# Kernel tuning notes

Hardware: AMD Instinct MI355X
Metric: run time of the kernel (lower is better)

The kernel has to match this reference:

```python
import jax, jax.numpy as jnp
import numpy as np

B, T, P, D, H = 4, 12, 196, 512, 8
DH = D // H
EPS = 1e-6


def _norm(x, alpha, bias):
    # torch Norm: alpha*(x-mean)/(std_unbiased+eps)+bias, std uses Bessel correction (ddof=1)
    mu = jnp.mean(x, axis=-1, keepdims=True)
    sd = jnp.std(x, axis=-1, ddof=1, keepdims=True)
    return alpha * (x - mu) / (sd + EPS) + bias


def setup_inputs() -> dict:
    key = jax.random.key(0)
    ks = jax.random.split(key, 12)
    s = 0.02

    def n(k, shape, scale=s):
        return jax.random.normal(k, shape, jnp.float32) * scale

    return {
        "x": jax.random.normal(ks[0], (B, T, P, D), jnp.float32),
        "Wq": n(ks[1], (D, D)), "bq": jnp.zeros((D,), jnp.float32),
        "Wk": n(ks[2], (D, D)), "bk": jnp.zeros((D,), jnp.float32),
        "Wv": n(ks[3], (D, D)), "bv": jnp.zeros((D,), jnp.float32),
        "in_a": jnp.ones((D,), jnp.float32), "in_b": jnp.zeros((D,), jnp.float32),
        "attn_a": jnp.ones((D,), jnp.float32), "attn_b": jnp.zeros((D,), jnp.float32),
        "out_a": jnp.ones((D,), jnp.float32), "out_b": jnp.zeros((D,), jnp.float32),
        "Wt": n(ks[4], (T, D, D)), "bt": jnp.zeros((T, D), jnp.float32),
        "pos": n(ks[5], (T, T, P, D), 0.02),
        "W1": n(ks[6], (2 * D, D)), "b1": jnp.zeros((2 * D,), jnp.float32),
        "W2": n(ks[7], (D, 2 * D)), "b2": jnp.zeros((D,), jnp.float32),
    }


def reference(x, Wq, bq, Wk, bk, Wv, bv, in_a, in_b, attn_a, attn_b,
              out_a, out_b, Wt, bt, pos, W1, b1, W2, b2):
    x2 = _norm(x, in_a, in_b)

    def proj(W, b):
        # [B,T,P,D] -> [B,T,H,P,DH]
        return (x2 @ W.T + b).reshape(B, T, P, H, DH).transpose(0, 1, 3, 2, 4)

    Q = proj(Wq, bq)
    K = proj(Wk, bk)
    V = proj(Wv, bv)

    # all-pairs temporal cross attention: [B,t,u,H,Pq,Pk]
    qk = jnp.einsum('btijk,builk->btuijl', Q, K) / np.sqrt(DH)
    attn = jax.nn.softmax(qk, axis=-1)  # no mask, dropout=0
    av = jnp.einsum('btuijl,builk->btuijk', attn, V)  # [B,t,u,H,P,DH]
    av = av.transpose(0, 1, 2, 4, 3, 5).reshape(B, T, T, P, D)
    av = _norm(av, attn_a, attn_b)
    x2p = av + pos  # pos broadcasts over batch

    # per-u Linear fused as one batched contraction, summed over u
    tc = jnp.einsum('btupd,ued->btpe', x2p / T, Wt) + jnp.sum(bt, axis=0)
    x = x + jax.nn.gelu(tc, approximate=False)

    x2 = _norm(x, out_a, out_b)
    h = jax.nn.gelu(x2 @ W1.T + b1, approximate=False)
    y = jax.nn.gelu(h @ W2.T + b2, approximate=False)
    return x + y
```

## Files before the change

kernel.cpp:

```cpp
#include <hip/hip_runtime.h>
#include <hip/hip_bf16.h>

typedef __hip_bfloat16 bf16;

typedef __bf16 bfrag8 __attribute__((ext_vector_type(8)));
typedef __bf16 bfrag4 __attribute__((ext_vector_type(4)));
typedef float  ffrag4 __attribute__((ext_vector_type(4)));
typedef float  ffrag16 __attribute__((ext_vector_type(16)));

#define EPS 1e-6f

__device__ __forceinline__ float gelu_exact(float v) {
  return 0.5f * v * (1.0f + erff(v * 0.7071067811865475f));
}

__device__ __forceinline__ void async16(const void* g, void* s) {
  __builtin_amdgcn_global_load_lds(
      (const __attribute__((address_space(1))) unsigned int*)g,
      (__attribute__((address_space(3))) unsigned int*)s, 16, 0, 0);
}

struct alignas(16) bf16x8 { bf16 v[8]; };
struct alignas(4)  bf16p2 { __bf16 v[2]; };

__global__ __launch_bounds__(256) void zero_acc_kernel(float* __restrict__ p) {
  size_t i = ((size_t)blockIdx.x * 256 + threadIdx.x) * 4;
  *(float4*)(p + i) = make_float4(0.f, 0.f, 0.f, 0.f);
}

__global__ __launch_bounds__(256) void conv_w_kernel(
    const float* __restrict__ Wq, const float* __restrict__ Wk,
    const float* __restrict__ Wv, const float* __restrict__ W1,
    const float* __restrict__ W2, const float* __restrict__ Wt,
    __bf16* __restrict__ dst)
{
  size_t e = ((size_t)blockIdx.x * 256 + threadIdx.x) * 8;
  const float* src; size_t off, dsto;
  if      (e <  262144) { src = Wq; off = e;           dsto = e; }
  else if (e <  524288) { src = Wk; off = e -  262144; dsto = e; }
  else if (e <  786432) { src = Wv; off = e -  524288; dsto = e; }
  else if (e < 1310720) { src = W1; off = e -  786432; dsto = e; }
  else if (e < 1835008) { src = W2; off = e - 1310720; dsto = e; }
  else if (e < 4980736) {
    src = Wt; off = e - 1835008;
    size_t u = off >> 18;
    size_t rem = off & 262143;
    size_t eo = rem >> 9, d = rem & 511;
    dsto = 1835008 + eo * 6144 + u * 512 + d;
  }
  else return;
  float4 f0 = *(const float4*)(src + off);
  float4 f1 = *(const float4*)(src + off + 4);
  bfrag8 o;
  o[0] = (__bf16)f0.x; o[1] = (__bf16)f0.y; o[2] = (__bf16)f0.z; o[3] = (__bf16)f0.w;
  o[4] = (__bf16)f1.x; o[5] = (__bf16)f1.y; o[6] = (__bf16)f1.z; o[7] = (__bf16)f1.w;
  *(bfrag8*)(dst + dsto) = o;
}

__global__ __launch_bounds__(512) void sum_bt_kernel(
    const float* __restrict__ bt, float* __restrict__ sbt)
{
  int n = threadIdx.x;
  float s = 0.f;
#pragma unroll
  for (int u = 0; u < 12; ++u) s += bt[u * 512 + n];
  sbt[n] = s;
}

__global__ __launch_bounds__(64) void norm_f32_to_bf16_kernel(
    const float* __restrict__ in, __bf16* __restrict__ out,
    const float* __restrict__ alpha, const float* __restrict__ beta)
{
  size_t row = blockIdx.x;
  int l = threadIdx.x;
  const float* r = in + row * 512 + l * 8;
  float4 v0 = *(const float4*)(r);
  float4 v1 = *(const float4*)(r + 4);
  float f[8] = {v0.x, v0.y, v0.z, v0.w, v1.x, v1.y, v1.z, v1.w};
  float s = 0.f, ss = 0.f;
#pragma unroll
  for (int q = 0; q < 8; ++q) { s += f[q]; ss += f[q] * f[q]; }
#pragma unroll
  for (int off = 32; off; off >>= 1) { s += __shfl_xor(s, off); ss += __shfl_xor(ss, off); }
  float mu = s * (1.f / 512.f);
  float var = fmaxf((ss - 512.f * mu * mu) * (1.f / 511.f), 0.f);
  float inv = 1.f / (sqrtf(var) + EPS);
  const float* al = alpha + l * 8;
  const float* be = beta + l * 8;
  float4 a0 = *(const float4*)al, a1 = *(const float4*)(al + 4);
  float4 b0 = *(const float4*)be, b1 = *(const float4*)(be + 4);
  float aa[8] = {a0.x, a0.y, a0.z, a0.w, a1.x, a1.y, a1.z, a1.w};
  float bb[8] = {b0.x, b0.y, b0.z, b0.w, b1.x, b1.y, b1.z, b1.w};
  bfrag8 o;
#pragma unroll
  for (int q = 0; q < 8; ++q) o[q] = (__bf16)(aa[q] * (f[q] - mu) * inv + bb[q]);
  *(bfrag8*)(out + row * 512 + l * 8) = o;
}

__global__ __launch_bounds__(256) void norm_av_kernel(
    bf16* __restrict__ av, const float* __restrict__ alpha,
    const float* __restrict__ beta, const float* __restrict__ pos)
{
  size_t row = (size_t)blockIdx.x * 4 + (threadIdx.x >> 6);
  int l = threadIdx.x & 63;
  bf16* r = av + row * 512 + (size_t)l * 8;
  bf16x8 ib = *(const bf16x8*)r;
  float f[8];
#pragma unroll
  for (int q = 0; q < 8; ++q) f[q] = __bfloat162float(ib.v[q]);
  float s = 0.f, ss = 0.f;
#pragma unroll
  for (int q = 0; q < 8; ++q) { s += f[q]; ss += f[q] * f[q]; }
#pragma unroll
  for (int off = 32; off; off >>= 1) { s += __shfl_xor(s, off); ss += __shfl_xor(ss, off); }
  float mu = s * (1.f / 512.f);
  float var = fmaxf((ss - 512.f * mu * mu) * (1.f / 511.f), 0.f);
  float inv = 1.f / (sqrtf(var) + EPS);
  size_t prow = row % 28224;
  const float* pr = pos + prow * 512 + l * 8;
  float4 p0 = *(const float4*)pr, p1 = *(const float4*)(pr + 4);
  const float* al = alpha + l * 8;
  const float* be = beta + l * 8;
  float4 a0 = *(const float4*)al, a1 = *(const float4*)(al + 4);
  float4 b0 = *(const float4*)be, b1 = *(const float4*)(be + 4);
  float pa[8] = {p0.x, p0.y, p0.z, p0.w, p1.x, p1.y, p1.z, p1.w};
  float aa[8] = {a0.x, a0.y, a0.z, a0.w, a1.x, a1.y, a1.z, a1.w};
  float bb[8] = {b0.x, b0.y, b0.z, b0.w, b1.x, b1.y, b1.z, b1.w};
  bf16x8 ob;
#pragma unroll
  for (int q = 0; q < 8; ++q)
    ob.v[q] = __float2bfloat16(aa[q] * (f[q] - mu) * inv + bb[q] + pa[q]);
  *(bf16x8*)r = ob;
}

__global__ __launch_bounds__(256) void mfma_nt_kernel(
    const __bf16* __restrict__ A,
    const __bf16* __restrict__ Bq, const __bf16* __restrict__ Bk,
    const __bf16* __restrict__ Bv,
    const float* __restrict__ bq, const float* __restrict__ bk,
    const float* __restrict__ bv,
    __bf16* __restrict__ oq, __bf16* __restrict__ ok, __bf16* __restrict__ ov,
    const float* __restrict__ res, float* __restrict__ fout,
    int K, int mode)
{
  __shared__ __bf16 As[128 * 32];
  __shared__ __bf16 Bs[128 * 32];
  int tid = threadIdx.x;
  int m0 = blockIdx.y * 128;
  int n0g = blockIdx.x * 128;

  const __bf16* Bsel; const float* biassel; __bf16* osel; int ncol0;
  if (mode == 0) {
    int sel = n0g >> 9;
    Bsel = sel == 0 ? Bq : (sel == 1 ? Bk : Bv);
    biassel = sel == 0 ? bq : (sel == 1 ? bk : bv);
    osel = sel == 0 ? oq : (sel == 1 ? ok : ov);
    ncol0 = n0g & 511;
  } else {
    Bsel = Bq; biassel = bq; osel = oq; ncol0 = n0g;
  }

  int srow = tid >> 2;
  int scol = ((tid & 3) ^ ((srow >> 1) & 3)) * 8;
  int rg0 = m0 + srow;       if (rg0 > 9407) rg0 = 9407;
  int rg1 = m0 + 64 + srow;  if (rg1 > 9407) rg1 = 9407;
  const __bf16* a0 = A + (size_t)rg0 * K + scol;
  const __bf16* a1 = A + (size_t)rg1 * K + scol;
  const __bf16* b0 = Bsel + (size_t)(ncol0 + srow) * K + scol;
  const __bf16* b1 = Bsel + (size_t)(ncol0 + 64 + srow) * K + scol;
  char* sa0 = (char*)As + tid * 16;
  char* sa1 = (char*)As + 4096 + tid * 16;
  char* sb0 = (char*)Bs + tid * 16;
  char* sb1 = (char*)Bs + 4096 + tid * 16;

  int l = tid & 63, w = tid >> 6;
  int lm = l & 15, lq = l >> 4;
  int wm = w >> 1, wn = w & 1;
  int rsw = ((((lm >> 1) & 3) ^ lq)) * 8;

  ffrag4 acc[4][4] = {};
  for (int k0 = 0; k0 < K; k0 += 32) {
    __syncthreads();
    async16(a0 + k0, sa0);
    async16(a1 + k0, sa1);
    async16(b0 + k0, sb0);
    async16(b1 + k0, sb1);
    __syncthreads();
    bfrag8 af[4], bfr[4];
#pragma unroll
    for (int i = 0; i < 4; ++i)
      af[i] = *(const bfrag8*)&As[(wm * 64 + i * 16 + lm) * 32 + rsw];
#pragma unroll
    for (int j = 0; j < 4; ++j)
      bfr[j] = *(const bfrag8*)&Bs[(wn * 64 + j * 16 + lm) * 32 + rsw];
#pragma unroll
    for (int i = 0; i < 4; ++i)
#pragma unroll
      for (int j = 0; j < 4; ++j)
        acc[i][j] = __builtin_amdgcn_mfma_f32_16x16x32_bf16(af[i], bfr[j], acc[i][j], 0, 0, 0);
  }

#pragma unroll
  for (int i = 0; i < 4; ++i) {
    int mbase = m0 + wm * 64 + i * 16 + lq * 4;
#pragma unroll
    for (int j = 0; j < 4; ++j) {
      int n = ncol0 + wn * 64 + j * 16 + lm;
      float bj = biassel[n];
#pragma unroll
      for (int r = 0; r < 4; ++r) {
        int mr = mbase + r;
        if (mr < 9408) {
          float v = acc[i][j][r] + bj;
          if (mode == 0)      osel[(size_t)mr * 512 + n] = (__bf16)v;
          else if (mode == 1) osel[(size_t)mr * 1024 + n] = (__bf16)gelu_exact(v);
          else                fout[(size_t)mr * 512 + n] =
                                res[(size_t)mr * 512 + n] + gelu_exact(v);
        }
      }
    }
  }
}

__global__ __launch_bounds__(256) void mfma_tc_kernel(
    const __bf16* __restrict__ X2p, const __bf16* __restrict__ Wte,
    float* __restrict__ accb)
{
  __shared__ __bf16 As[128 * 32];
  __shared__ __bf16 Bs[128 * 32];
  int tid = threadIdx.x;
  int m0 = blockIdx.y * 128;
  int n0 = blockIdx.x * 128;
  int z  = blockIdx.z;

  int srow = tid >> 2;
  int scol = ((tid & 3) ^ ((srow >> 1) & 3)) * 8;
  int rg0 = m0 + srow;       if (rg0 > 9407) rg0 = 9407;
  int rg1 = m0 + 64 + srow;  if (rg1 > 9407) rg1 = 9407;
  int btq0 = rg0 / 196, p0_ = rg0 - btq0 * 196;
  int btq1 = rg1 / 196, p1_ = rg1 - btq1 * 196;
  const __bf16* a0 = X2p + (size_t)btq0 * 1204224 + (size_t)p0_ * 512 + scol;
  const __bf16* a1 = X2p + (size_t)btq1 * 1204224 + (size_t)p1_ * 512 + scol;
  const __bf16* b0 = Wte + (size_t)(n0 + srow) * 6144 + scol;
  const __bf16* b1 = Wte + (size_t)(n0 + 64 + srow) * 6144 + scol;
  char* sa0 = (char*)As + tid * 16;
  char* sa1 = (char*)As + 4096 + tid * 16;
  char* sb0 = (char*)Bs + tid * 16;
  char* sb1 = (char*)Bs + 4096 + tid * 16;

  int l = tid & 63, w = tid >> 6;
  int lm = l & 15, lq = l >> 4;
  int wm = w >> 1, wn = w & 1;
  int rsw = ((((lm >> 1) & 3) ^ lq)) * 8;

  ffrag4 acc[4][4] = {};
  int kbeg = z * 1536, kend = kbeg + 1536;
  for (int k0 = kbeg; k0 < kend; k0 += 32) {
    size_t aoff = (size_t)(k0 >> 9) * 100352 + (size_t)(k0 & 511);
    __syncthreads();
    async16(a0 + aoff, sa0);
    async16(a1 + aoff, sa1);
    async16(b0 + k0, sb0);
    async16(b1 + k0, sb1);
    __syncthreads();
    bfrag8 af[4], bfr[4];
#pragma unroll
    for (int i = 0; i < 4; ++i)
      af[i] = *(const bfrag8*)&As[(wm * 64 + i * 16 + lm) * 32 + rsw];
#pragma unroll
    for (int j = 0; j < 4; ++j)
      bfr[j] = *(const bfrag8*)&Bs[(wn * 64 + j * 16 + lm) * 32 + rsw];
#pragma unroll
    for (int i = 0; i < 4; ++i)
#pragma unroll
      for (int j = 0; j < 4; ++j)
        acc[i][j] = __builtin_amdgcn_mfma_f32_16x16x32_bf16(af[i], bfr[j], acc[i][j], 0, 0, 0);
  }

#pragma unroll
  for (int i = 0; i < 4; ++i) {
    int mbase = m0 + wm * 64 + i * 16 + lq * 4;
#pragma unroll
    for (int j = 0; j < 4; ++j) {
      int n = n0 + wn * 64 + j * 16 + lm;
#pragma unroll
      for (int r = 0; r < 4; ++r) {
        int mr = mbase + r;
        if (mr < 9408)
          atomicAdd(accb + (size_t)mr * 512 + n, acc[i][j][r]);
      }
    }
  }
}

__global__ __launch_bounds__(64) void tc_epi_norm_kernel(
    const float* __restrict__ accb, const float* __restrict__ x,
    const float* __restrict__ sbt,
    const float* __restrict__ alpha, const float* __restrict__ beta,
    float* __restrict__ xmid, __bf16* __restrict__ x3b)
{
  size_t row = blockIdx.x;
  int l = threadIdx.x;
  size_t base = row * 512 + l * 8;
  float4 c0 = *(const float4*)(accb + base);
  float4 c1 = *(const float4*)(accb + base + 4);
  float4 x0 = *(const float4*)(x + base);
  float4 x1 = *(const float4*)(x + base + 4);
  float4 s0 = *(const float4*)(sbt + l * 8);
  float4 s1 = *(const float4*)(sbt + l * 8 + 4);
  float cc[8] = {c0.x, c0.y, c0.z, c0.w, c1.x, c1.y, c1.z, c1.w};
  float xx[8] = {x0.x, x0.y, x0.z, x0.w, x1.x, x1.y, x1.z, x1.w};
  float sv[8] = {s0.x, s0.y, s0.z, s0.w, s1.x, s1.y, s1.z, s1.w};
  float f[8];
#pragma unroll
  for (int q = 0; q < 8; ++q)
    f[q] = xx[q] + gelu_exact(cc[q] * (1.f / 12.f) + sv[q]);
  *(float4*)(xmid + base)     = make_float4(f[0], f[1], f[2], f[3]);
  *(float4*)(xmid + base + 4) = make_float4(f[4], f[5], f[6], f[7]);
  float s = 0.f, ss = 0.f;
#pragma unroll
  for (int q = 0; q < 8; ++q) { s += f[q]; ss += f[q] * f[q]; }
#pragma unroll
  for (int off = 32; off; off >>= 1) { s += __shfl_xor(s, off); ss += __shfl_xor(ss, off); }
  float mu = s * (1.f / 512.f);
  float var = fmaxf((ss - 512.f * mu * mu) * (1.f / 511.f), 0.f);
  float inv = 1.f / (sqrtf(var) + EPS);
  const float* al = alpha + l * 8;
  const float* be = beta + l * 8;
  float4 a0 = *(const float4*)al, a1 = *(const float4*)(al + 4);
  float4 b0 = *(const float4*)be, b1 = *(const float4*)(be + 4);
  float aa[8] = {a0.x, a0.y, a0.z, a0.w, a1.x, a1.y, a1.z, a1.w};
  float bb[8] = {b0.x, b0.y, b0.z, b0.w, b1.x, b1.y, b1.z, b1.w};
  bfrag8 o;
#pragma unroll
  for (int q = 0; q < 8; ++q) o[q] = (__bf16)(aa[q] * (f[q] - mu) * inv + bb[q]);
  *(bfrag8*)(x3b + base) = o;
}

__global__ __launch_bounds__(512, 4) void attn_kernel(
    const __bf16* __restrict__ Q, const __bf16* __restrict__ K,
    const __bf16* __restrict__ V, __bf16* __restrict__ av)
{
  __shared__ __bf16 Ks[196 * 64];
  __shared__ __bf16 Vt[64 * 208];
  __shared__ __bf16 Pball[8 * 32 * 20];

  int bid = blockIdx.x;
  int half = bid & 1;
  int h = (bid >> 1) & 7;
  int r0 = bid >> 4;
  int u = r0 % 12;
  int b = r0 / 12;

  const __bf16* Kp = K + ((size_t)(b * 12 + u) * 196) * 512 + h * 64;
  const __bf16* Vp = V + ((size_t)(b * 12 + u) * 196) * 512 + h * 64;

  for (int idx = threadIdx.x; idx < 196 * 8; idx += 512) {
    int r = idx >> 3, g = idx & 7;
    *(bfrag8*)&Ks[r * 64 + ((g ^ (r & 7)) * 8)] =
        *(const bfrag8*)&Kp[(size_t)r * 512 + g * 8];
  }
  for (int idx = threadIdx.x; idx < 64 * 6; idx += 512) {
    int r = idx / 6, c2 = 196 + (idx % 6) * 2;
    bf16p2 z; z.v[0] = (__bf16)0.f; z.v[1] = (__bf16)0.f;
    *(bf16p2*)&Vt[r * 208 + c2] = z;
  }
  for (int idx = threadIdx.x; idx < 98 * 8; idx += 512) {
    int r2 = (idx % 98) * 2, c8 = (idx / 98) * 8;
    bfrag8 va = *(const bfrag8*)&Vp[(size_t)r2 * 512 + c8];
    bfrag8 vb = *(const bfrag8*)&Vp[(size_t)(r2 + 1) * 512 + c8];
#pragma unroll
    for (int e = 0; e < 8; ++e) {
      bf16p2 pr; pr.v[0] = va[e]; pr.v[1] = vb[e];
      *(bf16p2*)&Vt[(c8 + e) * 208 + r2] = pr;
    }
  }
  __syncthreads();

  int w = threadIdx.x >> 6, l = threadIdx.x & 63;
  int l5 = l >> 5, c = l & 31;
  __bf16* Pb = Pball + w * (32 * 20);

  for (int unit = w; unit < 42; unit += 8) {
    int t = unit / 7, qt = unit - t * 7;
    int tq = half * 6 + t;
    const __bf16* Qp = Q + ((size_t)(b * 12 + tq) * 196) * 512 + h * 64;
    __bf16* avp = av + ((size_t)((b * 12 + tq) * 12 + u) * 196) * 512 + h * 64;
    int q0 = qt * 32;

    const __bf16* qp = Qp + (size_t)(q0 + c) * 512 + l5 * 8;
    bfrag8 qf[4];
    qf[0] = *(const bfrag8*)(qp);
    qf[1] = *(const bfrag8*)(qp + 16);
    qf[2] = *(const bfrag8*)(qp + 32);
    qf[3] = *(const bfrag8*)(qp + 48);

    ffrag16 O0, O1;
#pragma unroll
    for (int g = 0; g < 16; ++g) { O0[g] = 0.f; O1[g] = 0.f; }
    float sumacc = 0.f;

    for (int nt = 0; nt < 7; ++nt) {
      int key = nt * 32 + c; if (key > 195) key = 195;
      const __bf16* kbase = &Ks[key * 64];
      int kx = key & 7;

      ffrag16 s;
#pragma unroll
      for (int g = 0; g < 16; ++g) s[g] = 0.f;
#pragma unroll
      for (int kc = 0; kc < 4; ++kc) {
        bfrag8 kf = *(const bfrag8*)&kbase[(((kc * 2 + l5) ^ kx) * 8)];
        s = __builtin_amdgcn_mfma_f32_32x32x16_bf16(kf, qf[kc], s, 0, 0, 0);
      }

#pragma unroll
      for (int g = 0; g < 16; ++g) {
        float e = __expf(s[g] * 0.125f);
        bool keep = (nt < 6) || ((g < 4) && (l5 == 0));
        e = keep ? e : 0.f;
        s[g] = e;
        sumacc += e;
      }

#pragma unroll
      for (int sub = 0; sub < 2; ++sub) {
        if (nt == 6 && sub == 1) break;
#pragma unroll
        for (int g = 0; g < 8; ++g) {
          int gg = sub * 8 + g;
          int k16 = (gg & 3) + 8 * ((gg >> 2) & 1) + 4 * l5;
          Pb[c * 20 + k16] = (__bf16)s[gg];
        }
        __threadfence_block();
        int ch = nt * 2 + sub;
        bfrag4 plo = *(const bfrag4*)&Pb[c * 20 + l5 * 8];
        bfrag4 phi = *(const bfrag4*)&Pb[c * 20 + l5 * 8 + 4];
        bfrag8 pa = __builtin_shufflevector(plo, phi, 0, 1, 2, 3, 4, 5, 6, 7);
        bfrag8 v0 = *(const bfrag8*)&Vt[(size_t)(c     ) * 208 + ch * 16 + l5 * 8];
        bfrag8 v1 = *(const bfrag8*)&Vt[(size_t)(c + 32) * 208 + ch * 16 + l5 * 8];
        O0 = __builtin_amdgcn_mfma_f32_32x32x16_bf16(pa, v0, O0, 0, 0, 0);
        O1 = __builtin_amdgcn_mfma_f32_32x32x16_bf16(pa, v1, O1, 0, 0, 0);
      }
    }

    float stot = sumacc + __shfl_xor(sumacc, 32);

#pragma unroll
    for (int g = 0; g < 16; ++g) {
      int row = (g & 3) + 8 * (g >> 2) + 4 * l5;
      float sq = __shfl(stot, row);
      float iv = __builtin_amdgcn_rcpf(sq);
      int q = q0 + row;
      if (q < 196) {
        size_t base = (size_t)q * 512 + c;
        avp[base]      = (__bf16)(O0[g] * iv);
        avp[base + 32] = (__bf16)(O1[g] * iv);
      }
    }
  }
}

extern "C" void kernel_launch(void* const* d_in, const int* in_sizes, int n_in,
                              void* d_out, int out_size, void* d_ws, size_t ws_size,
                              hipStream_t stream)
{
  const float* x      = (const float*)d_in[0];
  const float* Wq     = (const float*)d_in[1];
  const float* bq     = (const float*)d_in[2];
  const float* Wk     = (const float*)d_in[3];
  const float* bk     = (const float*)d_in[4];
  const float* Wv     = (const float*)d_in[5];
  const float* bv     = (const float*)d_in[6];
  const float* in_a   = (const float*)d_in[7];
  const float* in_b   = (const float*)d_in[8];
  const float* attn_a = (const float*)d_in[9];
  const float* attn_b = (const float*)d_in[10];
  const float* out_a  = (const float*)d_in[11];
  const float* out_b  = (const float*)d_in[12];
  const float* Wt     = (const float*)d_in[13];
  const float* bt     = (const float*)d_in[14];
  const float* pos    = (const float*)d_in[15];
  const float* W1     = (const float*)d_in[16];
  const float* b1     = (const float*)d_in[17];
  const float* W2     = (const float*)d_in[18];
  const float* b2     = (const float*)d_in[19];

  char* ws = (char*)d_ws;
  const size_t bfb = (size_t)9408 * 512 * 2;
  __bf16* x2b  = (__bf16*)(ws);
  __bf16* Qb   = (__bf16*)(ws + bfb);
  __bf16* Kb   = (__bf16*)(ws + 2 * bfb);
  __bf16* Vb   = (__bf16*)(ws + 3 * bfb);
  __bf16* av   = (__bf16*)(ws + 4 * bfb);
  char*   wreg = ws + 4 * bfb + (size_t)115605504;
  __bf16* Wqb  = (__bf16*)(wreg);
  __bf16* Wkb  = (__bf16*)(wreg) + 262144;
  __bf16* Wvb  = (__bf16*)(wreg) + 524288;
  __bf16* W1b  = (__bf16*)(wreg) + 786432;
  __bf16* W2b  = (__bf16*)(wreg) + 1310720;
  __bf16* Wtb  = (__bf16*)(wreg) + 1835008;
  float*  sbt  = (float*)(wreg + 9961472);
  float*  accb = (float*)(wreg + 9963520);
  float*  xmid = (float*)(ws);
  __bf16* x3b  = (__bf16*)(ws + 2 * bfb);
  __bf16* hb   = (__bf16*)(ws + 4 * bfb);
  float*  out  = (float*)d_out;

  conv_w_kernel<<<2432, 256, 0, stream>>>(Wq, Wk, Wv, W1, W2, Wt, (__bf16*)wreg);
  sum_bt_kernel<<<1, 512, 0, stream>>>(bt, sbt);
  zero_acc_kernel<<<4704, 256, 0, stream>>>(accb);
  norm_f32_to_bf16_kernel<<<9408, 64, 0, stream>>>(x, x2b, in_a, in_b);
  mfma_nt_kernel<<<dim3(12, 74), 256, 0, stream>>>(
      x2b, Wqb, Wkb, Wvb, bq, bk, bv, Qb, Kb, Vb, nullptr, nullptr, 512, 0);
  attn_kernel<<<768, 512, 0, stream>>>(Qb, Kb, Vb, av);
  norm_av_kernel<<<28224, 256, 0, stream>>>((bf16*)av, attn_a, attn_b, pos);
  mfma_tc_kernel<<<dim3(4, 74, 4), 256, 0, stream>>>(av, Wtb, accb);
  tc_epi_norm_kernel<<<9408, 64, 0, stream>>>(accb, x, sbt, out_a, out_b, xmid, x3b);
  mfma_nt_kernel<<<dim3(8, 74), 256, 0, stream>>>(
      x3b, W1b, nullptr, nullptr, b1, nullptr, nullptr, hb, nullptr, nullptr,
      nullptr, nullptr, 512, 1);
  mfma_nt_kernel<<<dim3(4, 74), 256, 0, stream>>>(
      hb, W2b, nullptr, nullptr, b2, nullptr, nullptr, nullptr, nullptr, nullptr,
      xmid, out, 1024, 2);
}
```

Measured before the change: 571.2 us.

## Double-buffer LDS tiles and remap workgroups across XCDs in MFMA GEMM kernels

```diff
diff --git a/kernel.cpp b/kernel.cpp
--- a/kernel.cpp
+++ b/kernel.cpp
@@ -143,11 +143,18 @@
     const float* __restrict__ res, float* __restrict__ fout,
     int K, int mode)
 {
-  __shared__ __bf16 As[128 * 32];
-  __shared__ __bf16 Bs[128 * 32];
+  __shared__ __bf16 As[2 * 128 * 32];
+  __shared__ __bf16 Bs[2 * 128 * 32];
   int tid = threadIdx.x;
-  int m0 = blockIdx.y * 128;
-  int n0g = blockIdx.x * 128;
+
+  int nwg = gridDim.x * gridDim.y;
+  int cpx = nwg >> 3;
+  int lid = blockIdx.x + gridDim.x * blockIdx.y;
+  int logical = (lid & 7) * cpx + (lid >> 3);
+  int bx = logical % gridDim.x;
+  int by = logical / gridDim.x;
+  int m0 = by * 128;
+  int n0g = bx * 128;
 
   const __bf16* Bsel; const float* biassel; __bf16* osel; int ncol0;
   if (mode == 0) {
@@ -178,26 +185,39 @@
   int wm = w >> 1, wn = w & 1;
   int rsw = ((((lm >> 1) & 3) ^ lq)) * 8;
 
+  const int nsteps = K >> 5;
+  async16(a0, sa0);
+  async16(a1, sa1);
+  async16(b0, sb0);
+  async16(b1, sb1);
+  __syncthreads();
+
   ffrag4 acc[4][4] = {};
-  for (int k0 = 0; k0 < K; k0 += 32) {
-    __syncthreads();
-    async16(a0 + k0, sa0);
-    async16(a1 + k0, sa1);
-    async16(b0 + k0, sb0);
-    async16(b1 + k0, sb1);
-    __syncthreads();
+  int cur = 0;
+  for (int t = 0; t < nsteps; ++t) {
+    if (t + 1 < nsteps) {
+      int k1 = (t + 1) << 5;
+      int bo = (cur ^ 1) * 8192;
+      async16(a0 + k1, sa0 + bo);
+      async16(a1 + k1, sa1 + bo);
+      async16(b0 + k1, sb0 + bo);
+      async16(b1 + k1, sb1 + bo);
+    }
+    int co = cur * 4096;
     bfrag8 af[4], bfr[4];
 #pragma unroll
     for (int i = 0; i < 4; ++i)
-      af[i] = *(const bfrag8*)&As[(wm * 64 + i * 16 + lm) * 32 + rsw];
+      af[i] = *(const bfrag8*)&As[co + (wm * 64 + i * 16 + lm) * 32 + rsw];
 #pragma unroll
     for (int j = 0; j < 4; ++j)
-      bfr[j] = *(const bfrag8*)&Bs[(wn * 64 + j * 16 + lm) * 32 + rsw];
+      bfr[j] = *(const bfrag8*)&Bs[co + (wn * 64 + j * 16 + lm) * 32 + rsw];
 #pragma unroll
     for (int i = 0; i < 4; ++i)
 #pragma unroll
       for (int j = 0; j < 4; ++j)
         acc[i][j] = __builtin_amdgcn_mfma_f32_16x16x32_bf16(af[i], bfr[j], acc[i][j], 0, 0, 0);
+    __syncthreads();
+    cur ^= 1;
   }
 
 #pragma unroll
@@ -226,12 +246,20 @@
     const __bf16* __restrict__ X2p, const __bf16* __restrict__ Wte,
     float* __restrict__ accb)
 {
-  __shared__ __bf16 As[128 * 32];
-  __shared__ __bf16 Bs[128 * 32];
+  __shared__ __bf16 As[2 * 128 * 32];
+  __shared__ __bf16 Bs[2 * 128 * 32];
   int tid = threadIdx.x;
-  int m0 = blockIdx.y * 128;
-  int n0 = blockIdx.x * 128;
-  int z  = blockIdx.z;
+
+  int lid = blockIdx.x + 4 * (blockIdx.y + 74 * blockIdx.z);
+  int logical = (lid & 7) * 148 + (lid >> 3);
+  int lx = logical & 3;
+  int rest = logical >> 2;
+  int ly = rest % 74;
+  int lz = rest / 74;
+
+  int m0 = ly * 128;
+  int n0 = lx * 128;
+  int kbeg = lz * 1536;
 
   int srow = tid >> 2;
   int scol = ((tid & 3) ^ ((srow >> 1) & 3)) * 8;
@@ -253,28 +281,42 @@
   int wm = w >> 1, wn = w & 1;
   int rsw = ((((lm >> 1) & 3) ^ lq)) * 8;
 
-  ffrag4 acc[4][4] = {};
-  int kbeg = z * 1536, kend = kbeg + 1536;
-  for (int k0 = kbeg; k0 < kend; k0 += 32) {
-    size_t aoff = (size_t)(k0 >> 9) * 100352 + (size_t)(k0 & 511);
-    __syncthreads();
+  {
+    size_t aoff = (size_t)(kbeg >> 9) * 100352 + (size_t)(kbeg & 511);
     async16(a0 + aoff, sa0);
     async16(a1 + aoff, sa1);
-    async16(b0 + k0, sb0);
-    async16(b1 + k0, sb1);
-    __syncthreads();
+    async16(b0 + kbeg, sb0);
+    async16(b1 + kbeg, sb1);
+  }
+  __syncthreads();
+
+  ffrag4 acc[4][4] = {};
+  int cur = 0;
+  for (int t = 0; t < 48; ++t) {
+    if (t + 1 < 48) {
+      int k1 = kbeg + (t + 1) * 32;
+      size_t aoff = (size_t)(k1 >> 9) * 100352 + (size_t)(k1 & 511);
+      int bo = (cur ^ 1) * 8192;
+      async16(a0 + aoff, sa0 + bo);
+      async16(a1 + aoff, sa1 + bo);
+      async16(b0 + k1, sb0 + bo);
+      async16(b1 + k1, sb1 + bo);
+    }
+    int co = cur * 4096;
     bfrag8 af[4], bfr[4];
 #pragma unroll
     for (int i = 0; i < 4; ++i)
-      af[i] = *(const bfrag8*)&As[(wm * 64 + i * 16 + lm) * 32 + rsw];
+      af[i] = *(const bfrag8*)&As[co + (wm * 64 + i * 16 + lm) * 32 + rsw];
 #pragma unroll
     for (int j = 0; j < 4; ++j)
-      bfr[j] = *(const bfrag8*)&Bs[(wn * 64 + j * 16 + lm) * 32 + rsw];
+      bfr[j] = *(const bfrag8*)&Bs[co + (wn * 64 + j * 16 + lm) * 32 + rsw];
 #pragma unroll
     for (int i = 0; i < 4; ++i)
 #pragma unroll
       for (int j = 0; j < 4; ++j)
         acc[i][j] = __builtin_amdgcn_mfma_f32_16x16x32_bf16(af[i], bfr[j], acc[i][j], 0, 0, 0);
+    __syncthreads();
+    cur ^= 1;
   }
 
 #pragma unroll
```

After: 544.7 us. 4.6% less time.
